# Kernel tuning notes

Hardware: AMD Instinct MI355X
Metric: run time of the kernel (lower is better)

Reference implementation:

```python
import jax, jax.numpy as jnp
import numpy as np

EDGES = np.array([[0,6],[0,5],[6,8],[5,7],[0,62],[62,63],[63,64],[59,64],[59,60],[60,61],[61,62],[0,74],[71,72],[72,73],[73,74],[74,75],[75,76],[76,77],[77,78],[78,79],[79,80],[80,81],[81,82],[71,82],[71,83],[77,87],[83,84],[84,85],[85,86],[86,87],[87,88],[88,89],[89,90],[83,90],[0,65],[65,66],[66,67],[67,68],[68,69],[69,70],[65,70],[7,91],[91,92],[92,93],[93,94],[94,95],[91,96],[96,97],[97,98],[98,99],[91,100],[100,101],[101,102],[102,103],[91,104],[104,105],[105,106],[106,107],[91,108],[108,109],[109,110],[110,111],[8,112],[112,113],[113,114],[114,115],[115,116],[112,117],[117,118],[118,119],[119,120],[112,121],[121,122],[122,123],[123,124],[112,125],[125,126],[126,127],[127,128],[112,129],[129,130],[130,131],[131,132]], dtype=np.int32)
N_NODES = 102


def _gcn_structure():
    # Keep only edges whose endpoints fit in the 102-node feature view,
    # add self-loops, and compute symmetric GCN normalization (PyG gcn_norm).
    keep = (EDGES[:, 0] < N_NODES) & (EDGES[:, 1] < N_NODES)
    e = EDGES[keep]
    row, col = e[:, 0], e[:, 1]
    loops = np.arange(N_NODES, dtype=np.int32)
    row_f = np.concatenate([row, loops])
    col_f = np.concatenate([col, loops])
    deg = np.zeros(N_NODES, dtype=np.float32)
    np.add.at(deg, col_f, 1.0)  # in-degree incl. self-loop
    dinv = 1.0 / np.sqrt(np.maximum(deg, 1.0))
    norm = (dinv[row_f] * dinv[col_f]).astype(np.float32)
    return row_f, col_f, norm

_ROW, _COL, _NORM = _gcn_structure()


def setup_inputs() -> dict:
    key = jax.random.key(0)
    ks = jax.random.split(key, 5)
    B = 8192
    return {
        "x": jax.random.normal(ks[0], (B, 204), dtype=jnp.float32),
        "W_gcn": jax.random.normal(ks[1], (2, 64), dtype=jnp.float32) * 0.5,
        "b_gcn": jax.random.normal(ks[2], (64,), dtype=jnp.float32) * 0.1,
        "W_proj": jax.random.normal(ks[3], (64, 128), dtype=jnp.float32) * 0.1,
        "b_proj": jax.random.normal(ks[4], (128,), dtype=jnp.float32) * 0.1,
    }


def reference(x, W_gcn, b_gcn, W_proj, b_proj):
    B = x.shape[0]
    xn = x.reshape(B, N_NODES, 2)                      # (B, 102, 2)
    h = jnp.einsum('bni,ih->bnh', xn, W_gcn)           # GCN linear: (B, 102, H)
    norm = jnp.asarray(_NORM)
    msgs = h[:, _ROW, :] * norm[None, :, None]         # gather + normalize: (B, E+N, H)
    agg = jnp.zeros_like(h).at[:, _COL, :].add(msgs)   # scatter-add into targets
    agg = agg + b_gcn                                  # GCN bias
    act = jax.nn.relu(agg)                             # activation
    out = jnp.einsum('bnh,he->bne', act, W_proj) + b_proj  # projection: (B, 102, 128)
    return out
```

## Files before the change

### kernel.cpp

```cpp
#include <hip/hip_runtime.h>
#include <hip/hip_bf16.h>

#define NN   102
#define NE   83
#define NPAD 128

using bf16x8 = __attribute__((ext_vector_type(8))) short;
using f32x4  = __attribute__((ext_vector_type(4))) float;

__device__ __constant__ int EDGES_C[NE * 2] = {
    0,6, 0,5, 6,8, 5,7, 0,62, 62,63, 63,64, 59,64, 59,60, 60,61, 61,62,
    0,74, 71,72, 72,73, 73,74, 74,75, 75,76, 76,77, 77,78, 78,79, 79,80,
    80,81, 81,82, 71,82, 71,83, 77,87, 83,84, 84,85, 85,86, 86,87, 87,88,
    88,89, 89,90, 83,90, 0,65, 65,66, 66,67, 67,68, 68,69, 69,70, 65,70,
    7,91, 91,92, 92,93, 93,94, 94,95, 91,96, 96,97, 97,98, 98,99, 91,100,
    100,101, 101,102, 102,103, 91,104, 104,105, 105,106, 106,107, 91,108,
    108,109, 109,110, 110,111, 8,112, 112,113, 113,114, 114,115, 115,116,
    112,117, 117,118, 118,119, 119,120, 112,121, 121,122, 122,123, 123,124,
    112,125, 125,126, 126,127, 127,128, 112,129, 129,130, 130,131, 131,132
};

#define WS_BFRAG 0
#define WS_OFF   16384
#define WS_ER    (16384 + 512)
#define WS_EN    (16384 + 512 + 1024)

__device__ inline unsigned short f2bf(float f) {
  union { float f; unsigned u; } v; v.f = f;
  unsigned r = v.u + 0x7fffu + ((v.u >> 16) & 1u);
  return (unsigned short)(r >> 16);
}

__device__ inline unsigned cvt_pk_bf16(float lo, float hi) {
  unsigned r;
  asm("v_cvt_pk_bf16_f32 %0, %1, %2" : "=v"(r) : "v"(lo), "v"(hi));
  return r;
}

__global__ void gnn_setup(const float* __restrict__ Wp, char* __restrict__ ws) {
  __shared__ float s_dinv[NN];
  __shared__ int   s_cnt[NN];
  __shared__ int   s_off[NN + 1];
  const int t = threadIdx.x;

  if (t < NN) {
    int deg = 1, cnt = 1;
    for (int e = 0; e < NE; ++e) {
      int r = EDGES_C[2*e], c = EDGES_C[2*e+1];
      if (r < NN && c == t) { ++deg; ++cnt; }
    }
    s_dinv[t] = 1.0f / sqrtf((float)deg);
    s_cnt[t]  = cnt;
  }
  __syncthreads();
  if (t < NN) {
    int o = 0;
    for (int c = 0; c < t; ++c) o += s_cnt[c];
    s_off[t] = o;
    if (t == NN - 1) s_off[NN] = o + s_cnt[t];
  }
  __syncthreads();
  int*   off = (int*)(ws + WS_OFF);
  int*   er  = (int*)(ws + WS_ER);
  float* en  = (float*)(ws + WS_EN);
  if (t < NN) {
    int c = t, pos = s_off[c];
    float dc = s_dinv[c];
    er[pos] = c; en[pos] = dc * dc; ++pos;
    for (int e = 0; e < NE; ++e) {
      int r = EDGES_C[2*e], cc = EDGES_C[2*e+1];
      if (r < NN && cc == c) { er[pos] = r; en[pos] = s_dinv[r] * dc; ++pos; }
    }
    off[c] = s_off[c];
    if (c == 0) off[NN] = s_off[NN];
  }
  unsigned short* bf = (unsigned short*)(ws + WS_BFRAG);
  for (int idx = t; idx < 16 * 64; idx += blockDim.x) {
    int lane = idx & 63;
    int f    = idx >> 6;
    int mt   = f >> 1, kc = f & 1;
    int e    = mt * 16 + (lane & 15);
    int kb   = kc * 32 + (lane >> 4) * 8;
    unsigned short* dst = bf + idx * 8;
#pragma unroll
    for (int i = 0; i < 8; ++i) dst[i] = f2bf(Wp[(kb + i) * 128 + e]);
  }
}

__global__ __launch_bounds__(256) void gnn_main(
    const float* __restrict__ x, const float* __restrict__ Wg,
    const float* __restrict__ bg, const float* __restrict__ bp,
    const char* __restrict__ ws, float* __restrict__ out, int B) {
  const int t    = threadIdx.x;
  const int lane = t & 63;
  const int wv   = t >> 6;
  const int b    = blockIdx.x * 4 + wv;

  __shared__ float swg[128];
  __shared__ float sbg[64];
  __shared__ float sbp[128];
  __shared__ float sxw[4][208];
  __shared__ float syw[4][NPAD][2];
  __shared__ float st[4][16][132];

  if (t < 128) { swg[t] = Wg[t]; sbp[t] = bp[t]; }
  if (t < 64)  sbg[t] = bg[t];
  __syncthreads();

  if (b >= B) return;

  float* sx = sxw[wv];
  float (*sy)[2] = syw[wv];

  if (lane < 51)
    *(f32x4*)&sx[lane * 4] = *(const f32x4*)(x + (size_t)b * 204 + lane * 4);

  {
    const int*   off = (const int*)(ws + WS_OFF);
    const int*   er  = (const int*)(ws + WS_ER);
    const float* en  = (const float*)(ws + WS_EN);
#pragma unroll
    for (int half = 0; half < 2; ++half) {
      const int n = lane + half * 64;
      float y0 = 0.f, y1 = 0.f;
      if (n < NN) {
        int s = off[n], e2 = off[n + 1];
        for (int j = s; j < e2; ++j) {
          int r = er[j]; float w = en[j];
          y0 = fmaf(w, sx[2 * r],     y0);
          y1 = fmaf(w, sx[2 * r + 1], y1);
        }
      }
      sy[n][0] = y0; sy[n][1] = y1;
    }
  }

  const int l15 = lane & 15;
  const int lhi = lane >> 4;
  const int kb  = lhi * 8;
  const int rb  = lhi * 4;
  const int c32 = (lane & 31) * 4;
  const int rhi = lane >> 5;

  const bf16x8* bfr = (const bf16x8*)(ws + WS_BFRAG);
  bf16x8 Apf[8][2];
#pragma unroll
  for (int mt = 0; mt < 8; ++mt) {
    Apf[mt][0] = bfr[(mt * 2 + 0) * 64 + lane];
    Apf[mt][1] = bfr[(mt * 2 + 1) * 64 + lane];
  }
  f32x4 bias[8];
#pragma unroll
  for (int mt = 0; mt < 8; ++mt)
    bias[mt] = *(const f32x4*)&sbp[mt * 16 + rb];

  float* ob = out + (size_t)b * (NN * 128);

  for (int nt = 0; nt < 7; ++nt) {
    const int node = nt * 16 + l15;
    const float y0 = sy[node][0], y1 = sy[node][1];
    bf16x8 Bact[2];
#pragma unroll
    for (int kc = 0; kc < 2; ++kc) {
      float v[8];
#pragma unroll
      for (int i = 0; i < 8; ++i) {
        int h = kc * 32 + kb + i;
        float a = fmaf(y0, swg[h], fmaf(y1, swg[64 + h], sbg[h]));
        v[i] = fmaxf(a, 0.f);
      }
      union { unsigned u[4]; bf16x8 f; } pk;
      pk.u[0] = cvt_pk_bf16(v[0], v[1]);
      pk.u[1] = cvt_pk_bf16(v[2], v[3]);
      pk.u[2] = cvt_pk_bf16(v[4], v[5]);
      pk.u[3] = cvt_pk_bf16(v[6], v[7]);
      Bact[kc] = pk.f;
    }

    f32x4 acc[8];
#pragma unroll
    for (int mt = 0; mt < 8; ++mt) acc[mt] = bias[mt];
#pragma unroll
    for (int mt = 0; mt < 8; ++mt)
#pragma unroll
      for (int kc = 0; kc < 2; ++kc)
        acc[mt] = __builtin_amdgcn_mfma_f32_16x16x32_bf16(
            Apf[mt][kc], Bact[kc], acc[mt], 0, 0, 0);

#pragma unroll
    for (int mt = 0; mt < 8; ++mt)
      *(f32x4*)&st[wv][l15][mt * 16 + rb] = acc[mt];

    const int rows = (nt < 6) ? 16 : (NN - 96);
#pragma unroll
    for (int pass = 0; pass < 8; ++pass) {
      const int n2 = pass * 2 + rhi;
      if (n2 < rows) {
        f32x4 row = *(const f32x4*)&st[wv][n2][c32];
        *(f32x4*)(ob + (nt * 16 + n2) * 128 + c32) = row;
      }
    }
  }
}

extern "C" void kernel_launch(void* const* d_in, const int* in_sizes, int n_in,
                              void* d_out, int out_size, void* d_ws, size_t ws_size,
                              hipStream_t stream) {
  const float* x  = (const float*)d_in[0];
  const float* Wg = (const float*)d_in[1];
  const float* bg = (const float*)d_in[2];
  const float* Wp = (const float*)d_in[3];
  const float* bp = (const float*)d_in[4];
  float* out = (float*)d_out;
  const int B = in_sizes[0] / 204;

  gnn_setup<<<1, 256, 0, stream>>>(Wp, (char*)d_ws);
  gnn_main<<<(B + 3) / 4, 256, 0, stream>>>(x, Wg, bg, bp, (const char*)d_ws, out, B);
}
```

Measured before the change: 108.9 us.

## Software-pipeline MFMA tiles with output stores, hoist GCN weights to registers

The per-tile loop is restructured so the MFMA compute of tile nt runs before the LDS read-back and global store of tile nt-1, letting the stores overlap the next tile's math. GCN weight and bias values move from repeated LDS reads into registers, and the projection bias is added at store time instead of seeding the accumulators. The setup kernel now splits the bf16 fragment conversion into a second block so it runs alongside the CSR build. This raises register pressure, and the single per-wave LDS slab is reused across stages, which relies on in-wave ordering for correctness.

```diff
diff --git a/kernel.cpp b/kernel.cpp
--- a/kernel.cpp
+++ b/kernel.cpp
@@ -38,10 +38,26 @@
 }
 
 __global__ void gnn_setup(const float* __restrict__ Wp, char* __restrict__ ws) {
+  const int t = threadIdx.x;
+
+  if (blockIdx.x != 0) {
+    unsigned short* bf = (unsigned short*)(ws + WS_BFRAG);
+    for (int idx = t; idx < 16 * 64; idx += 256) {
+      int lane = idx & 63;
+      int f    = idx >> 6;
+      int mt   = f >> 1, kc = f & 1;
+      int e    = mt * 16 + (lane & 15);
+      int kb   = kc * 32 + (lane >> 4) * 8;
+      unsigned short* dst = bf + idx * 8;
+#pragma unroll
+      for (int i = 0; i < 8; ++i) dst[i] = f2bf(Wp[(kb + i) * 128 + e]);
+    }
+    return;
+  }
+
   __shared__ float s_dinv[NN];
   __shared__ int   s_cnt[NN];
   __shared__ int   s_off[NN + 1];
-  const int t = threadIdx.x;
 
   if (t < NN) {
     int deg = 1, cnt = 1;
@@ -73,17 +89,6 @@
     }
     off[c] = s_off[c];
     if (c == 0) off[NN] = s_off[NN];
-  }
-  unsigned short* bf = (unsigned short*)(ws + WS_BFRAG);
-  for (int idx = t; idx < 16 * 64; idx += blockDim.x) {
-    int lane = idx & 63;
-    int f    = idx >> 6;
-    int mt   = f >> 1, kc = f & 1;
-    int e    = mt * 16 + (lane & 15);
-    int kb   = kc * 32 + (lane >> 4) * 8;
-    unsigned short* dst = bf + idx * 8;
-#pragma unroll
-    for (int i = 0; i < 8; ++i) dst[i] = f2bf(Wp[(kb + i) * 128 + e]);
   }
 }
 
@@ -142,6 +147,17 @@
   const int c32 = (lane & 31) * 4;
   const int rhi = lane >> 5;
 
+  f32x4 WG0[2][2], WG1[2][2], BG[2][2];
+#pragma unroll
+  for (int kc = 0; kc < 2; ++kc)
+#pragma unroll
+    for (int h2 = 0; h2 < 2; ++h2) {
+      WG0[kc][h2] = *(const f32x4*)&swg[kc * 32 + kb + 4 * h2];
+      WG1[kc][h2] = *(const f32x4*)&swg[64 + kc * 32 + kb + 4 * h2];
+      BG[kc][h2]  = *(const f32x4*)&sbg[kc * 32 + kb + 4 * h2];
+    }
+  const f32x4 bpv = *(const f32x4*)&sbp[c32];
+
   const bf16x8* bfr = (const bf16x8*)(ws + WS_BFRAG);
   bf16x8 Apf[8][2];
 #pragma unroll
@@ -149,14 +165,12 @@
     Apf[mt][0] = bfr[(mt * 2 + 0) * 64 + lane];
     Apf[mt][1] = bfr[(mt * 2 + 1) * 64 + lane];
   }
-  f32x4 bias[8];
-#pragma unroll
-  for (int mt = 0; mt < 8; ++mt)
-    bias[mt] = *(const f32x4*)&sbp[mt * 16 + rb];
 
   float* ob = out + (size_t)b * (NN * 128);
 
-  for (int nt = 0; nt < 7; ++nt) {
+  f32x4 acc[8];
+
+  auto compute_tile = [&](int nt) {
     const int node = nt * 16 + l15;
     const float y0 = sy[node][0], y1 = sy[node][1];
     bf16x8 Bact[2];
@@ -165,8 +179,8 @@
       float v[8];
 #pragma unroll
       for (int i = 0; i < 8; ++i) {
-        int h = kc * 32 + kb + i;
-        float a = fmaf(y0, swg[h], fmaf(y1, swg[64 + h], sbg[h]));
+        float a = fmaf(y0, WG0[kc][i >> 2][i & 3],
+                  fmaf(y1, WG1[kc][i >> 2][i & 3], BG[kc][i >> 2][i & 3]));
         v[i] = fmaxf(a, 0.f);
       }
       union { unsigned u[4]; bf16x8 f; } pk;
@@ -176,31 +190,43 @@
       pk.u[3] = cvt_pk_bf16(v[6], v[7]);
       Bact[kc] = pk.f;
     }
-
-    f32x4 acc[8];
-#pragma unroll
-    for (int mt = 0; mt < 8; ++mt) acc[mt] = bias[mt];
+#pragma unroll
+    for (int mt = 0; mt < 8; ++mt) { f32x4 z = {0.f,0.f,0.f,0.f}; acc[mt] = z; }
 #pragma unroll
     for (int mt = 0; mt < 8; ++mt)
 #pragma unroll
       for (int kc = 0; kc < 2; ++kc)
         acc[mt] = __builtin_amdgcn_mfma_f32_16x16x32_bf16(
             Apf[mt][kc], Bact[kc], acc[mt], 0, 0, 0);
-
+  };
+
+  auto write_slab = [&]() {
 #pragma unroll
     for (int mt = 0; mt < 8; ++mt)
       *(f32x4*)&st[wv][l15][mt * 16 + rb] = acc[mt];
-
-    const int rows = (nt < 6) ? 16 : (NN - 96);
+  };
+
+  auto read_store = [&](int nt, int rows) {
 #pragma unroll
     for (int pass = 0; pass < 8; ++pass) {
       const int n2 = pass * 2 + rhi;
       if (n2 < rows) {
         f32x4 row = *(const f32x4*)&st[wv][n2][c32];
+        row = row + bpv;
         *(f32x4*)(ob + (nt * 16 + n2) * 128 + c32) = row;
       }
     }
-  }
+  };
+
+  compute_tile(0);
+  write_slab();
+#pragma unroll
+  for (int nt = 1; nt < 7; ++nt) {
+    compute_tile(nt);
+    read_store(nt - 1, 16);
+    write_slab();
+  }
+  read_store(6, NN - 96);
 }
 
 extern "C" void kernel_launch(void* const* d_in, const int* in_sizes, int n_in,
@@ -214,6 +240,6 @@
   float* out = (float*)d_out;
   const int B = in_sizes[0] / 204;
 
-  gnn_setup<<<1, 256, 0, stream>>>(Wp, (char*)d_ws);
+  gnn_setup<<<2, 256, 0, stream>>>(Wp, (char*)d_ws);
   gnn_main<<<(B + 3) / 4, 256, 0, stream>>>(x, Wg, bg, bp, (const char*)d_ws, out, B);
 }
```

Measured after the change: 110.3 us. About the same (+1.3%).
